# Optimization experiments

Measured on AMD Instinct MI355X. Metric: run time of the kernel, lower is better.

Reference implementation:

```python
import jax, jax.numpy as jnp
import numpy as np

B, S, E = 64, 512, 1024   # batch, seq_len, enc_size (bert-large hidden)
P, K, C = 200, 10, 3      # num_prototypes, proto_size, num_classes


def setup_inputs() -> dict:
    key = jax.random.key(0)
    k1, k2, k3 = jax.random.split(key, 3)
    embedding = jax.random.normal(k1, (B, S, E), dtype=jnp.float32)
    # protolayer initialized with nn.init.uniform_ -> U[0,1)
    protolayer = jax.random.uniform(k2, (P, K, E), dtype=jnp.float32)
    fc_weight = jax.random.normal(k3, (C, P), dtype=jnp.float32) * 0.05
    return {"embedding": embedding, "protolayer": protolayer, "fc_weight": fc_weight}


def reference(embedding, protolayer, fc_weight):
    # torch.cdist(embedding[:,None], protolayer, p=2) broadcasts to [B,P,S,K]:
    # distances[b,p,s,k] = ||embedding[b,s,:] - protolayer[p,k,:]||_2
    x2 = jnp.sum(embedding * embedding, axis=-1)            # [B,S]
    y2 = jnp.sum(protolayer * protolayer, axis=-1)          # [P,K]
    xy = jnp.einsum('bse,pke->bpsk', embedding, protolayer) # [B,P,S,K]
    d2 = x2[:, None, :, None] + y2[None, :, None, :] - 2.0 * xy
    distances = jnp.sqrt(jnp.maximum(d2, 0.0))              # [B,P,S,K]
    # -max_pool2d(-d, kernel=(S,1)) == min over seq dim
    min_distances = jnp.min(distances, axis=2)               # [B,P,K]
    prototype_distances = jnp.mean(min_distances, axis=-1)   # [B,P]
    class_out = prototype_distances @ fc_weight.T            # [B,C]
    return prototype_distances, distances, class_out
```

## Files before the change

### kernel.cpp

```cpp
#include <hip/hip_runtime.h>
#include <hip/hip_bf16.h>

#define B_ 64
#define S_ 512
#define E_ 1024
#define P_ 200
#define K_ 10
#define C_ 3

#define BM 128
#define BN 128
#define BKS 64
#define NSTAGE (E_ / BKS)
#define NROWS_A (B_ * S_)
#define NROWS_B (P_ * K_)
#define NB_PAD 2048
#define NROWS_P (NROWS_A + NB_PAD)
#define NMT 256
#define NNT 16

typedef __attribute__((ext_vector_type(8))) short short8;
typedef __attribute__((ext_vector_type(4))) float f32x4;
typedef __attribute__((ext_vector_type(16))) float f32x16;

__device__ __forceinline__ float bf2f(unsigned short u) {
    unsigned int x = ((unsigned int)u) << 16;
    return __uint_as_float(x);
}
__device__ __forceinline__ unsigned short f2bf(float f) {
    __hip_bfloat16 h = __float2bfloat16(f);
    unsigned short u;
    __builtin_memcpy(&u, &h, 2);
    return u;
}

__device__ __forceinline__ int swz(int row, int kbyte) {
    return (row * (BKS * 2) + kbyte) ^ ((row & 7) << 4);
}

#define GLDS16(gsrc, ldst)                                                              \
    __builtin_amdgcn_global_load_lds((const __attribute__((address_space(1))) unsigned int*)(gsrc), \
                                     (__attribute__((address_space(3))) unsigned int*)(ldst), 16, 0, 0)

__global__ __launch_bounds__(256) void preconvert(const float* __restrict__ emb,
                                                  const float* __restrict__ proto,
                                                  unsigned short* __restrict__ bf,
                                                  float* __restrict__ xy2) {
    const int row  = blockIdx.x * 4 + (threadIdx.x >> 6);
    const int lane = threadIdx.x & 63;
    unsigned short* dst = bf + (size_t)row * E_;

    if (row >= NROWS_A + NROWS_B) {
        ushort4 z = {0, 0, 0, 0};
#pragma unroll
        for (int p = 0; p < 4; ++p) *(ushort4*)(dst + p * 256 + lane * 4) = z;
        if (lane == 0) xy2[row] = 0.f;
        return;
    }
    const float* src = (row < NROWS_A) ? emb + (size_t)row * E_
                                       : proto + (size_t)(row - NROWS_A) * E_;
    float s = 0.f;
#pragma unroll
    for (int p = 0; p < 4; ++p) {
        float4 v = *(const float4*)(src + p * 256 + lane * 4);
        ushort4 h = { f2bf(v.x), f2bf(v.y), f2bf(v.z), f2bf(v.w) };
        float a = bf2f(h.x), b = bf2f(h.y), c = bf2f(h.z), d = bf2f(h.w);
        s += a * a + b * b + c * c + d * d;
        *(ushort4*)(dst + p * 256 + lane * 4) = h;
    }
#pragma unroll
    for (int off = 32; off > 0; off >>= 1) s += __shfl_xor(s, off);
    if (lane == 0) xy2[row] = s;
}

__global__ __launch_bounds__(256) void dist_gemm_bf(const unsigned short* __restrict__ Abf,
                                                    const unsigned short* __restrict__ Bbf,
                                                    const float* __restrict__ x2g,
                                                    const float* __restrict__ y2g,
                                                    float* __restrict__ dist,
                                                    float* __restrict__ ws_min) {
    __shared__ unsigned short As[2][BM * BKS];
    __shared__ unsigned short Bs[2][BN * BKS];
    __shared__ float red[2][BN];

    const int tid  = threadIdx.x;
    const int lane = tid & 63;
    const int wv   = tid >> 6;
    const int wr   = wv >> 1;
    const int wc   = wv & 1;
    const int l31  = lane & 31;
    const int hi   = lane >> 5;

    const int id = blockIdx.x;
    const int sw = (id & 7) * (4096 / 8) + (id >> 3);
    const int nt = sw & (NNT - 1);
    const int mt = sw >> 4;

    const unsigned short* aSrc[4];
    const unsigned short* bSrc[4];
    unsigned lOff[4];
#pragma unroll
    for (int i = 0; i < 4; ++i) {
        int idx = i * 256 + tid;
        int r = idx >> 3, c = idx & 7;
        aSrc[i] = Abf + (size_t)(mt * BM + r) * E_ + (c ^ (r & 7)) * 8;
        bSrc[i] = Bbf + (size_t)(nt * BN + r) * E_ + (c ^ (r & 7)) * 8;
        lOff[i] = (unsigned)(i * 256 + wv * 64) * 8;
    }

    f32x16 acc[2][2];
#pragma unroll
    for (int i = 0; i < 2; ++i)
#pragma unroll
        for (int j = 0; j < 2; ++j)
#pragma unroll
            for (int r = 0; r < 16; ++r) acc[i][j][r] = 0.f;

#define ISSUE(tt, bb)                                                          \
    do {                                                                       \
        const size_t ko_ = (size_t)(tt) * BKS;                                 \
        _Pragma("unroll")                                                      \
        for (int i_ = 0; i_ < 4; ++i_) {                                       \
            GLDS16(aSrc[i_] + ko_, &As[bb][lOff[i_]]);                         \
            GLDS16(bSrc[i_] + ko_, &Bs[bb][lOff[i_]]);                         \
        }                                                                      \
    } while (0)

#define COMPUTE(bb)                                                            \
    do {                                                                       \
        const char* Ab_ = (const char*)As[bb];                                 \
        const char* Bb_ = (const char*)Bs[bb];                                 \
        _Pragma("unroll")                                                      \
        for (int kk = 0; kk < 4; ++kk) {                                       \
            const int kbyte = kk * 32 + hi * 16;                               \
            short8 af[2], bfr[2];                                              \
            _Pragma("unroll")                                                  \
            for (int mf = 0; mf < 2; ++mf)                                     \
                af[mf] = *(const short8*)(Ab_ + swz(wr * 64 + mf * 32 + l31, kbyte)); \
            _Pragma("unroll")                                                  \
            for (int nf = 0; nf < 2; ++nf)                                     \
                bfr[nf] = *(const short8*)(Bb_ + swz(wc * 64 + nf * 32 + l31, kbyte)); \
            _Pragma("unroll")                                                  \
            for (int mf = 0; mf < 2; ++mf)                                     \
                _Pragma("unroll")                                              \
                for (int nf = 0; nf < 2; ++nf)                                 \
                    acc[mf][nf] = __builtin_amdgcn_mfma_f32_32x32x16_bf16(     \
                        af[mf], bfr[nf], acc[mf][nf], 0, 0, 0);                \
        }                                                                      \
    } while (0)

    ISSUE(0, 0);
    __syncthreads();

    int buf = 0;
    for (int t = 0; t < NSTAGE; ++t) {
        if (t + 1 < NSTAGE) ISSUE(t + 1, buf ^ 1);
        COMPUTE(buf);
        __syncthreads();
        buf ^= 1;
    }

    float y2v[2];
#pragma unroll
    for (int nf = 0; nf < 2; ++nf)
        y2v[nf] = y2g[nt * BN + wc * 64 + nf * 32 + l31];

    float mloc[2];
    mloc[0] = 3.4e38f; mloc[1] = 3.4e38f;

#pragma unroll
    for (int mf = 0; mf < 2; ++mf) {
        float x2v[16];
#pragma unroll
        for (int rg = 0; rg < 16; ++rg) {
            int row_l = (rg & 3) + 8 * (rg >> 2) + 4 * hi;
            x2v[rg] = x2g[mt * BM + wr * 64 + mf * 32 + row_l];
        }
#pragma unroll
        for (int nf = 0; nf < 2; ++nf) {
            int n = nt * BN + wc * 64 + nf * 32 + l31;
            int p = n / K_;
            int k = n - p * K_;
            bool valid = (n < NROWS_B);
#pragma unroll
            for (int rg = 0; rg < 16; ++rg) {
                int row_l = (rg & 3) + 8 * (rg >> 2) + 4 * hi;
                int m = mt * BM + wr * 64 + mf * 32 + row_l;
                int b = m >> 9;
                int s = m & (S_ - 1);
                float d2 = x2v[rg] + y2v[nf] - 2.f * acc[mf][nf][rg];
                float d  = sqrtf(fmaxf(d2, 0.f));
                if (valid) dist[(((size_t)b * P_ + p) * S_ + s) * K_ + k] = d;
                mloc[nf] = fminf(mloc[nf], d);
            }
        }
    }

#pragma unroll
    for (int nf = 0; nf < 2; ++nf)
        mloc[nf] = fminf(mloc[nf], __shfl_xor(mloc[nf], 32));
    if (hi == 0) {
#pragma unroll
        for (int nf = 0; nf < 2; ++nf)
            red[wr][wc * 64 + nf * 32 + l31] = mloc[nf];
    }
    __syncthreads();
    if (tid < BN) {
        float v = fminf(red[0][tid], red[1][tid]);
        ws_min[(size_t)mt * NB_PAD + nt * BN + tid] = v;
    }
#undef ISSUE
#undef COMPUTE
}

__global__ __launch_bounds__(256) void mean_fc(const float* __restrict__ ws_min,
                                               const float* __restrict__ fcw,
                                               float* __restrict__ pd,
                                               float* __restrict__ cls) {
    const int b = blockIdx.x;
    const int t = threadIdx.x;
    __shared__ float pds[P_];
    if (t < P_) {
        float sum = 0.f;
#pragma unroll
        for (int k = 0; k < K_; ++k) {
            float m = 3.4e38f;
#pragma unroll
            for (int st = 0; st < 4; ++st)
                m = fminf(m, ws_min[(size_t)(b * 4 + st) * NB_PAD + t * K_ + k]);
            sum += m;
        }
        float v = sum * (1.0f / K_);
        pd[b * P_ + t] = v;
        pds[t] = v;
    }
    __syncthreads();
    if (t < C_) {
        float s = 0.f;
        for (int p = 0; p < P_; ++p) s += pds[p] * fcw[t * P_ + p];
        cls[b * C_ + t] = s;
    }
}

#define FBM 128
#define FBN 80
__device__ __forceinline__ int swzf(int row, int kbyte) {
    return (row * (BKS * 2) + kbyte) ^ ((row & 7) << 4);
}
__global__ __launch_bounds__(256) void dist_mfma_fb(const float* __restrict__ emb,
                                                    const float* __restrict__ proto,
                                                    float* __restrict__ dist) {
    __shared__ short As[FBM * BKS];
    __shared__ short Bs[FBN * BKS];
    __shared__ float x2s[FBM];
    __shared__ float y2s[FBN];

    const int tid  = threadIdx.x;
    const int lane = tid & 63;
    const int wv   = tid >> 6;
    const int l15  = lane & 15;
    const int lh   = lane >> 4;

    const int id = blockIdx.x;
    const int sw = (id & 7) * (6400 / 8) + (id >> 3);
    const int nt = sw % 25;
    const int mt = sw / 25;

    const float* Ab = emb + (size_t)mt * FBM * E_ + (size_t)(tid >> 4) * E_ + (tid & 15) * 4;
    const float* Bb = proto + (size_t)nt * FBN * E_ + (size_t)(tid >> 4) * E_ + (tid & 15) * 4;

    f32x4 acc[2][5];
#pragma unroll
    for (int i = 0; i < 2; ++i)
#pragma unroll
        for (int j = 0; j < 5; ++j) acc[i][j] = (f32x4){0.f, 0.f, 0.f, 0.f};

    float x2p[8], y2p[5];
#pragma unroll
    for (int i = 0; i < 8; ++i) x2p[i] = 0.f;
#pragma unroll
    for (int i = 0; i < 5; ++i) y2p[i] = 0.f;

    float4 pa[8], pb[5];
#pragma unroll
    for (int i = 0; i < 8; ++i) pa[i] = *(const float4*)(Ab + (size_t)i * 16 * E_);
#pragma unroll
    for (int i = 0; i < 5; ++i) pb[i] = *(const float4*)(Bb + (size_t)i * 16 * E_);

    for (int t = 0; t < NSTAGE; ++t) {
        ushort4 ca[8];
#pragma unroll
        for (int i = 0; i < 8; ++i) {
            float4 v = pa[i];
            x2p[i] += v.x * v.x + v.y * v.y + v.z * v.z + v.w * v.w;
            ca[i] = (ushort4){ f2bf(v.x), f2bf(v.y), f2bf(v.z), f2bf(v.w) };
        }
        ushort4 cb[5];
#pragma unroll
        for (int i = 0; i < 5; ++i) {
            float4 v = pb[i];
            y2p[i] += v.x * v.x + v.y * v.y + v.z * v.z + v.w * v.w;
            cb[i] = (ushort4){ f2bf(v.x), f2bf(v.y), f2bf(v.z), f2bf(v.w) };
        }
        __syncthreads();
#pragma unroll
        for (int i = 0; i < 8; ++i) {
            int idx = i * 256 + tid;
            *(ushort4*)((char*)As + swzf(idx >> 4, (idx & 15) * 8)) = ca[i];
        }
#pragma unroll
        for (int i = 0; i < 5; ++i) {
            int idx = i * 256 + tid;
            *(ushort4*)((char*)Bs + swzf(idx >> 4, (idx & 15) * 8)) = cb[i];
        }
        __syncthreads();
        if (t + 1 < NSTAGE) {
            const float* An = Ab + (size_t)(t + 1) * BKS;
            const float* Bn = Bb + (size_t)(t + 1) * BKS;
#pragma unroll
            for (int i = 0; i < 8; ++i) pa[i] = *(const float4*)(An + (size_t)i * 16 * E_);
#pragma unroll
            for (int i = 0; i < 5; ++i) pb[i] = *(const float4*)(Bn + (size_t)i * 16 * E_);
        }
#pragma unroll
        for (int kk = 0; kk < 2; ++kk) {
            const int kbyte = kk * 64 + lh * 16;
            short8 af[2];
#pragma unroll
            for (int mf = 0; mf < 2; ++mf)
                af[mf] = *(const short8*)((const char*)As + swzf(wv * 32 + mf * 16 + l15, kbyte));
            short8 bfr[5];
#pragma unroll
            for (int nf = 0; nf < 5; ++nf)
                bfr[nf] = *(const short8*)((const char*)Bs + swzf(nf * 16 + l15, kbyte));
#pragma unroll
            for (int mf = 0; mf < 2; ++mf)
#pragma unroll
                for (int nf = 0; nf < 5; ++nf)
                    acc[mf][nf] = __builtin_amdgcn_mfma_f32_16x16x32_bf16(
                        af[mf], bfr[nf], acc[mf][nf], 0, 0, 0);
        }
    }

#pragma unroll
    for (int i = 0; i < 8; ++i) {
        float v = x2p[i];
        v += __shfl_xor(v, 1); v += __shfl_xor(v, 2);
        v += __shfl_xor(v, 4); v += __shfl_xor(v, 8);
        if (l15 == 0) x2s[16 * i + (tid >> 4)] = v;
    }
#pragma unroll
    for (int i = 0; i < 5; ++i) {
        float v = y2p[i];
        v += __shfl_xor(v, 1); v += __shfl_xor(v, 2);
        v += __shfl_xor(v, 4); v += __shfl_xor(v, 8);
        if (l15 == 0) y2s[16 * i + (tid >> 4)] = v;
    }
    __syncthreads();

#pragma unroll
    for (int mf = 0; mf < 2; ++mf) {
#pragma unroll
        for (int nf = 0; nf < 5; ++nf) {
#pragma unroll
            for (int rg = 0; rg < 4; ++rg) {
                int ml = wv * 32 + mf * 16 + lh * 4 + rg;
                int nl = nf * 16 + l15;
                int m = mt * FBM + ml;
                int n = nt * FBN + nl;
                int b = m >> 9;
                int s = m & (S_ - 1);
                int p = n / K_;
                int k = n - p * K_;
                float d2 = x2s[ml] + y2s[nl] - 2.f * acc[mf][nf][rg];
                dist[(((size_t)b * P_ + p) * S_ + s) * K_ + k] = sqrtf(fmaxf(d2, 0.f));
            }
        }
    }
}

__global__ __launch_bounds__(256) void min_mean(const float* __restrict__ dist,
                                                float* __restrict__ pd) {
    const int p = blockIdx.x;
    const int b = blockIdx.y;
    const float* dp = dist + ((size_t)b * P_ + p) * (size_t)(S_ * K_);
    const int tid = threadIdx.x;

    const float4* base = (const float4*)(dp + (size_t)tid * 20);
    float4 q0 = base[0], q1 = base[1], q2 = base[2], q3 = base[3], q4 = base[4];

    float mn[K_];
    mn[0] = fminf(q0.x, q2.z); mn[1] = fminf(q0.y, q2.w);
    mn[2] = fminf(q0.z, q3.x); mn[3] = fminf(q0.w, q3.y);
    mn[4] = fminf(q1.x, q3.z); mn[5] = fminf(q1.y, q3.w);
    mn[6] = fminf(q1.z, q4.x); mn[7] = fminf(q1.w, q4.y);
    mn[8] = fminf(q2.x, q4.z); mn[9] = fminf(q2.y, q4.w);

#pragma unroll
    for (int k = 0; k < K_; ++k) {
#pragma unroll
        for (int off = 32; off > 0; off >>= 1)
            mn[k] = fminf(mn[k], __shfl_xor(mn[k], off));
    }

    __shared__ float red[4][K_];
    if ((tid & 63) == 0) {
#pragma unroll
        for (int k = 0; k < K_; ++k) red[tid >> 6][k] = mn[k];
    }
    __syncthreads();
    if (tid == 0) {
        float sum = 0.f;
#pragma unroll
        for (int k = 0; k < K_; ++k)
            sum += fminf(fminf(red[0][k], red[1][k]), fminf(red[2][k], red[3][k]));
        pd[b * P_ + p] = sum * (1.0f / K_);
    }
}

__global__ void fc_kernel(const float* __restrict__ pd, const float* __restrict__ fc,
                          float* __restrict__ cls) {
    int tid = threadIdx.x;
    if (tid < B_ * C_) {
        int b = tid / C_;
        int c = tid % C_;
        float s = 0.f;
        for (int p = 0; p < P_; ++p) s += pd[b * P_ + p] * fc[c * P_ + p];
        cls[b * C_ + c] = s;
    }
}

extern "C" void kernel_launch(void* const* d_in, const int* in_sizes, int n_in,
                              void* d_out, int out_size, void* d_ws, size_t ws_size,
                              hipStream_t stream) {
    const float* emb   = (const float*)d_in[0];
    const float* proto = (const float*)d_in[1];
    const float* fc    = (const float*)d_in[2];
    float* out = (float*)d_out;

    float* pd   = out;
    float* dist = out + (size_t)B_ * P_;
    float* cls  = out + (size_t)B_ * P_ + (size_t)B_ * P_ * S_ * K_;

    const size_t bf_bytes  = (size_t)NROWS_P * E_ * 2;
    const size_t xy2_bytes = (size_t)NROWS_P * 4;
    const size_t min_bytes = (size_t)NMT * NB_PAD * 4;
    const size_t ws_need   = bf_bytes + xy2_bytes + min_bytes;

    if (ws_size >= ws_need) {
        unsigned short* bf = (unsigned short*)d_ws;
        float* xy2    = (float*)((char*)d_ws + bf_bytes);
        float* ws_min = (float*)((char*)d_ws + bf_bytes + xy2_bytes);
        preconvert<<<NROWS_P / 4, 256, 0, stream>>>(emb, proto, bf, xy2);
        dist_gemm_bf<<<NMT * NNT, 256, 0, stream>>>(bf, bf + (size_t)NROWS_A * E_,
                                                    xy2, xy2 + NROWS_A, dist, ws_min);
        mean_fc<<<B_, 256, 0, stream>>>(ws_min, fc, pd, cls);
    } else {
        dist_mfma_fb<<<6400, 256, 0, stream>>>(emb, proto, dist);
        min_mean<<<dim3(P_, B_), 256, 0, stream>>>(dist, pd);
        fc_kernel<<<1, 256, 0, stream>>>(pd, fc, cls);
    }
}
```

Before: 287.5 us.

## Interleave global-to-LDS prefetch with MFMA phases using barriers and setprio

Restructures the GEMM main loop into four phases per K-stage. Each phase loads LDS fragments, issues one slice of the next stage's global-to-LDS loads, then runs the MFMAs at raised wave priority, with an s_barrier between the load and compute parts. The loop is unrolled by two so buffer indices are compile-time constants, and explicit vmcnt waits replace __syncthreads. The aim is to spread memory issue across compute and keep MFMA work from different waves in step, at the cost of more barriers per stage.

```diff
diff --git a/kernel.cpp b/kernel.cpp
--- a/kernel.cpp
+++ b/kernel.cpp
@@ -116,49 +116,62 @@
 #pragma unroll
             for (int r = 0; r < 16; ++r) acc[i][j][r] = 0.f;
 
-#define ISSUE(tt, bb)                                                          \
-    do {                                                                       \
-        const size_t ko_ = (size_t)(tt) * BKS;                                 \
-        _Pragma("unroll")                                                      \
-        for (int i_ = 0; i_ < 4; ++i_) {                                       \
-            GLDS16(aSrc[i_] + ko_, &As[bb][lOff[i_]]);                         \
-            GLDS16(bSrc[i_] + ko_, &Bs[bb][lOff[i_]]);                         \
-        }                                                                      \
-    } while (0)
-
-#define COMPUTE(bb)                                                            \
+#define PHASE(bb, f, doIssue, tt)                                              \
     do {                                                                       \
         const char* Ab_ = (const char*)As[bb];                                 \
         const char* Bb_ = (const char*)Bs[bb];                                 \
+        const int kbyte = (f) * 32 + hi * 16;                                  \
+        short8 af[2], bfr[2];                                                  \
         _Pragma("unroll")                                                      \
-        for (int kk = 0; kk < 4; ++kk) {                                       \
-            const int kbyte = kk * 32 + hi * 16;                               \
-            short8 af[2], bfr[2];                                              \
-            _Pragma("unroll")                                                  \
-            for (int mf = 0; mf < 2; ++mf)                                     \
-                af[mf] = *(const short8*)(Ab_ + swz(wr * 64 + mf * 32 + l31, kbyte)); \
+        for (int mf = 0; mf < 2; ++mf)                                         \
+            af[mf] = *(const short8*)(Ab_ + swz(wr * 64 + mf * 32 + l31, kbyte)); \
+        _Pragma("unroll")                                                      \
+        for (int nf = 0; nf < 2; ++nf)                                         \
+            bfr[nf] = *(const short8*)(Bb_ + swz(wc * 64 + nf * 32 + l31, kbyte)); \
+        if (doIssue) {                                                         \
+            const size_t ko_ = (size_t)(tt) * BKS;                             \
+            GLDS16(aSrc[f] + ko_, &As[(bb) ^ 1][lOff[f]]);                     \
+            GLDS16(bSrc[f] + ko_, &Bs[(bb) ^ 1][lOff[f]]);                     \
+        }                                                                      \
+        __builtin_amdgcn_sched_barrier(0);                                     \
+        __builtin_amdgcn_s_barrier();                                          \
+        __builtin_amdgcn_s_setprio(1);                                         \
+        _Pragma("unroll")                                                      \
+        for (int mf = 0; mf < 2; ++mf)                                         \
             _Pragma("unroll")                                                  \
             for (int nf = 0; nf < 2; ++nf)                                     \
-                bfr[nf] = *(const short8*)(Bb_ + swz(wc * 64 + nf * 32 + l31, kbyte)); \
-            _Pragma("unroll")                                                  \
-            for (int mf = 0; mf < 2; ++mf)                                     \
-                _Pragma("unroll")                                              \
-                for (int nf = 0; nf < 2; ++nf)                                 \
-                    acc[mf][nf] = __builtin_amdgcn_mfma_f32_32x32x16_bf16(     \
-                        af[mf], bfr[nf], acc[mf][nf], 0, 0, 0);                \
-        }                                                                      \
+                acc[mf][nf] = __builtin_amdgcn_mfma_f32_32x32x16_bf16(         \
+                    af[mf], bfr[nf], acc[mf][nf], 0, 0, 0);                    \
+        __builtin_amdgcn_s_setprio(0);                                         \
     } while (0)
 
-    ISSUE(0, 0);
-    __syncthreads();
-
-    int buf = 0;
-    for (int t = 0; t < NSTAGE; ++t) {
-        if (t + 1 < NSTAGE) ISSUE(t + 1, buf ^ 1);
-        COMPUTE(buf);
-        __syncthreads();
-        buf ^= 1;
-    }
+#define STAGE(bb, tt)                                                          \
+    do {                                                                       \
+        const bool doIssue_ = ((tt) + 1) < NSTAGE;                             \
+        PHASE(bb, 0, doIssue_, (tt) + 1);                                      \
+        PHASE(bb, 1, doIssue_, (tt) + 1);                                      \
+        PHASE(bb, 2, doIssue_, (tt) + 1);                                      \
+        PHASE(bb, 3, doIssue_, (tt) + 1);                                      \
+        if (doIssue_) { asm volatile("s_waitcnt vmcnt(0)" ::: "memory"); }     \
+        __builtin_amdgcn_s_barrier();                                          \
+        __builtin_amdgcn_sched_barrier(0);                                     \
+    } while (0)
+
+#pragma unroll
+    for (int i = 0; i < 4; ++i) {
+        GLDS16(aSrc[i], &As[0][lOff[i]]);
+        GLDS16(bSrc[i], &Bs[0][lOff[i]]);
+    }
+    asm volatile("s_waitcnt vmcnt(0)" ::: "memory");
+    __builtin_amdgcn_s_barrier();
+    __builtin_amdgcn_sched_barrier(0);
+
+    for (int t2 = 0; t2 < NSTAGE; t2 += 2) {
+        STAGE(0, t2);
+        STAGE(1, t2 + 1);
+    }
+#undef PHASE
+#undef STAGE
 
     float y2v[2];
 #pragma unroll
@@ -209,8 +222,6 @@
         float v = fminf(red[0][tid], red[1][tid]);
         ws_min[(size_t)mt * NB_PAD + nt * BN + tid] = v;
     }
-#undef ISSUE
-#undef COMPUTE
 }
 
 __global__ __launch_bounds__(256) void mean_fc(const float* __restrict__ ws_min,
```

Result: slower. 326.8 us (+13.7%).

## Halve GEMM K-stage depth, reorganize LDS layout, and raise occupancy hint

Applied to the files above, without the earlier changes.

The bf16 distance GEMM now loads 32-wide K slices per stage instead of 64, which halves its LDS footprint. The shared-memory tile uses a new blocked layout of 8-row by 16-byte groups in place of the XOR swizzle, and the direct global-to-LDS load mapping is rewritten to match. A launch_bounds minimum of 4 blocks per CU is added to raise occupancy. The trade is twice as many barriers and K iterations in exchange for more resident waves, with possible register pressure or bank conflicts from the new layout. The fallback kernel keeps its 64-wide stages under its own constants.

```diff
diff --git a/kernel.cpp b/kernel.cpp
--- a/kernel.cpp
+++ b/kernel.cpp
@@ -10,7 +10,7 @@
 
 #define BM 128
 #define BN 128
-#define BKS 64
+#define BKS 32
 #define NSTAGE (E_ / BKS)
 #define NROWS_A (B_ * S_)
 #define NROWS_B (P_ * K_)
@@ -34,8 +34,8 @@
     return u;
 }
 
-__device__ __forceinline__ int swz(int row, int kbyte) {
-    return (row * (BKS * 2) + kbyte) ^ ((row & 7) << 4);
+__device__ __forceinline__ int lda(int row, int kbyte) {
+    return ((row >> 3) << 9) + ((kbyte >> 4) << 7) + ((row & 7) << 4) + (kbyte & 15);
 }
 
 #define GLDS16(gsrc, ldst)                                                              \
@@ -73,12 +73,12 @@
     if (lane == 0) xy2[row] = s;
 }
 
-__global__ __launch_bounds__(256) void dist_gemm_bf(const unsigned short* __restrict__ Abf,
-                                                    const unsigned short* __restrict__ Bbf,
-                                                    const float* __restrict__ x2g,
-                                                    const float* __restrict__ y2g,
-                                                    float* __restrict__ dist,
-                                                    float* __restrict__ ws_min) {
+__global__ __launch_bounds__(256, 4) void dist_gemm_bf(const unsigned short* __restrict__ Abf,
+                                                       const unsigned short* __restrict__ Bbf,
+                                                       const float* __restrict__ x2g,
+                                                       const float* __restrict__ y2g,
+                                                       float* __restrict__ dist,
+                                                       float* __restrict__ ws_min) {
     __shared__ unsigned short As[2][BM * BKS];
     __shared__ unsigned short Bs[2][BN * BKS];
     __shared__ float red[2][BN];
@@ -96,16 +96,17 @@
     const int nt = sw & (NNT - 1);
     const int mt = sw >> 4;
 
-    const unsigned short* aSrc[4];
-    const unsigned short* bSrc[4];
-    unsigned lOff[4];
-#pragma unroll
-    for (int i = 0; i < 4; ++i) {
-        int idx = i * 256 + tid;
-        int r = idx >> 3, c = idx & 7;
-        aSrc[i] = Abf + (size_t)(mt * BM + r) * E_ + (c ^ (r & 7)) * 8;
-        bSrc[i] = Bbf + (size_t)(nt * BN + r) * E_ + (c ^ (r & 7)) * 8;
-        lOff[i] = (unsigned)(i * 256 + wv * 64) * 8;
+    const unsigned short* aSrc[2];
+    const unsigned short* bSrc[2];
+    unsigned lOff[2];
+#pragma unroll
+    for (int i = 0; i < 2; ++i) {
+        int j = i * 4 + wv;
+        int row = j * 16 + ((lane >> 5) << 3) + (lane & 7);
+        int chunk = (lane >> 3) & 3;
+        aSrc[i] = Abf + (size_t)(mt * BM + row) * E_ + chunk * 8;
+        bSrc[i] = Bbf + (size_t)(nt * BN + row) * E_ + chunk * 8;
+        lOff[i] = (unsigned)j * 512;
     }
 
     f32x16 acc[2][2];
@@ -120,7 +121,7 @@
     do {                                                                       \
         const size_t ko_ = (size_t)(tt) * BKS;                                 \
         _Pragma("unroll")                                                      \
-        for (int i_ = 0; i_ < 4; ++i_) {                                       \
+        for (int i_ = 0; i_ < 2; ++i_) {                                       \
             GLDS16(aSrc[i_] + ko_, &As[bb][lOff[i_]]);                         \
             GLDS16(bSrc[i_] + ko_, &Bs[bb][lOff[i_]]);                         \
         }                                                                      \
@@ -131,15 +132,15 @@
         const char* Ab_ = (const char*)As[bb];                                 \
         const char* Bb_ = (const char*)Bs[bb];                                 \
         _Pragma("unroll")                                                      \
-        for (int kk = 0; kk < 4; ++kk) {                                       \
+        for (int kk = 0; kk < 2; ++kk) {                                       \
             const int kbyte = kk * 32 + hi * 16;                               \
             short8 af[2], bfr[2];                                              \
             _Pragma("unroll")                                                  \
             for (int mf = 0; mf < 2; ++mf)                                     \
-                af[mf] = *(const short8*)(Ab_ + swz(wr * 64 + mf * 32 + l31, kbyte)); \
+                af[mf] = *(const short8*)(Ab_ + lda(wr * 64 + mf * 32 + l31, kbyte)); \
             _Pragma("unroll")                                                  \
             for (int nf = 0; nf < 2; ++nf)                                     \
-                bfr[nf] = *(const short8*)(Bb_ + swz(wc * 64 + nf * 32 + l31, kbyte)); \
+                bfr[nf] = *(const short8*)(Bb_ + lda(wc * 64 + nf * 32 + l31, kbyte)); \
             _Pragma("unroll")                                                  \
             for (int mf = 0; mf < 2; ++mf)                                     \
                 _Pragma("unroll")                                              \
@@ -159,6 +160,8 @@
         __syncthreads();
         buf ^= 1;
     }
+#undef ISSUE
+#undef COMPUTE
 
     float y2v[2];
 #pragma unroll
@@ -209,8 +212,6 @@
         float v = fminf(red[0][tid], red[1][tid]);
         ws_min[(size_t)mt * NB_PAD + nt * BN + tid] = v;
     }
-#undef ISSUE
-#undef COMPUTE
 }
 
 __global__ __launch_bounds__(256) void mean_fc(const float* __restrict__ ws_min,
@@ -244,14 +245,16 @@
 
 #define FBM 128
 #define FBN 80
+#define FBKS 64
+#define FNST 16
 __device__ __forceinline__ int swzf(int row, int kbyte) {
-    return (row * (BKS * 2) + kbyte) ^ ((row & 7) << 4);
+    return (row * (FBKS * 2) + kbyte) ^ ((row & 7) << 4);
 }
 __global__ __launch_bounds__(256) void dist_mfma_fb(const float* __restrict__ emb,
                                                     const float* __restrict__ proto,
                                                     float* __restrict__ dist) {
-    __shared__ short As[FBM * BKS];
-    __shared__ short Bs[FBN * BKS];
+    __shared__ short As[FBM * FBKS];
+    __shared__ short Bs[FBN * FBKS];
     __shared__ float x2s[FBM];
     __shared__ float y2s[FBN];
 
@@ -287,7 +290,7 @@
 #pragma unroll
     for (int i = 0; i < 5; ++i) pb[i] = *(const float4*)(Bb + (size_t)i * 16 * E_);
 
-    for (int t = 0; t < NSTAGE; ++t) {
+    for (int t = 0; t < FNST; ++t) {
         ushort4 ca[8];
 #pragma unroll
         for (int i = 0; i < 8; ++i) {
@@ -314,9 +317,9 @@
             *(ushort4*)((char*)Bs + swzf(idx >> 4, (idx & 15) * 8)) = cb[i];
         }
         __syncthreads();
-        if (t + 1 < NSTAGE) {
-            const float* An = Ab + (size_t)(t + 1) * BKS;
-            const float* Bn = Bb + (size_t)(t + 1) * BKS;
+        if (t + 1 < FNST) {
+            const float* An = Ab + (size_t)(t + 1) * FBKS;
+            const float* Bn = Bb + (size_t)(t + 1) * FBKS;
 #pragma unroll
             for (int i = 0; i < 8; ++i) pa[i] = *(const float4*)(An + (size_t)i * 16 * E_);
 #pragma unroll
```

New measurement: 332.7 us. 15.7% more time.
